# Optimization experiments

Hardware: AMD Instinct MI355X
Metric: run time of the kernel (lower is better)

The kernel has to match this reference:

```python
import jax, jax.numpy as jnp
import numpy as np

N = 50000          # nodes
E = 1600000        # edges (avg degree 32)
F_IN = 64          # input feature dim
SIZES = (64, 64)   # GATConv output sizes, heads=1
C_OUT = 5          # classifier classes
G = 64             # number of graphs in batch
SLOPE = 0.2        # LeakyReLU negative slope (PyG GATConv default)


def _glorot(key, shape):
    fan_in, fan_out = shape[0], shape[-1]
    s = jnp.sqrt(2.0 / (fan_in + fan_out)).astype(jnp.float32)
    return jax.random.normal(key, shape, jnp.float32) * s


def setup_inputs() -> dict:
    key = jax.random.key(0)
    ks = jax.random.split(key, 16)
    x = jax.random.normal(ks[0], (N, F_IN), jnp.float32)
    edge_index = jax.random.randint(ks[1], (2, E), 0, N)
    batch = jnp.sort(jax.random.randint(ks[2], (N,), 0, G))
    # layer 1 params
    W1 = _glorot(ks[3], (F_IN, SIZES[0]))
    a1s = _glorot(ks[4], (SIZES[0],))
    a1d = _glorot(ks[5], (SIZES[0],))
    b1 = jnp.zeros((SIZES[0],), jnp.float32)
    # layer 2 params
    W2 = _glorot(ks[6], (SIZES[0], SIZES[1]))
    a2s = _glorot(ks[7], (SIZES[1],))
    a2d = _glorot(ks[8], (SIZES[1],))
    b2 = jnp.zeros((SIZES[1],), jnp.float32)
    # final linear
    Wl = _glorot(ks[9], (SIZES[1], C_OUT))
    bl = jnp.zeros((C_OUT,), jnp.float32)
    return {"x": x, "edge_index": edge_index, "batch": batch,
            "W1": W1, "a1s": a1s, "a1d": a1d, "b1": b1,
            "W2": W2, "a2s": a2s, "a2d": a2d, "b2": b2,
            "Wl": Wl, "bl": bl}


def _gat_conv(h_in, W, a_src, a_dst, b, src, dst):
    # PyG GATConv, heads=1: h = W x; e_ij = LeakyReLU(a_src.h_j + a_dst.h_i)
    # alpha = softmax over edges grouped by destination i; out_i = sum alpha*h_j + b
    h = h_in @ W                                   # [N, F]
    e = jax.nn.leaky_relu((h @ a_src)[src] + (h @ a_dst)[dst], SLOPE)  # [E']
    m = jax.ops.segment_max(e, dst, num_segments=N)
    p = jnp.exp(e - m[dst])
    z = jax.ops.segment_sum(p, dst, num_segments=N)
    alpha = p / z[dst]                             # [E']
    out = jax.ops.segment_sum(h[src] * alpha[:, None], dst, num_segments=N)
    return out + b


def reference(x, edge_index, batch, W1, a1s, a1d, b1, W2, a2s, a2d, b2, Wl, bl):
    # add self-loops (PyG GATConv default add_self_loops=True)
    loop = jnp.arange(N, dtype=edge_index.dtype)
    src = jnp.concatenate([edge_index[0], loop])
    dst = jnp.concatenate([edge_index[1], loop])
    h = jax.nn.relu(_gat_conv(x, W1, a1s, a1d, b1, src, dst))
    h = jax.nn.relu(_gat_conv(h, W2, a2s, a2d, b2, src, dst))
    # global max pool per graph
    g = jax.ops.segment_max(h, batch, num_segments=G)   # [G, F]
    # dropout(p=0.3) is identity in eval mode
    return g @ Wl + bl
```

## Files before the change

### kernel.cpp

```cpp
#include <hip/hip_runtime.h>
#include <hip/hip_fp16.h>

#define N_NODES 50000
#define N_EDGES 1600000
#define F 64
#define G_GRAPHS 64
#define C_CLS 5
#define SLOPE 0.2f

#define NBUCKET ((N_NODES + 127) >> 7)
#define ACHUNK 4096
#define NCHUNKS ((N_EDGES + ACHUNK - 1) / ACHUNK)
#define CAP 8192
#define MAXCH 4
#define XPAD 68

__device__ __forceinline__ float lrelu(float x) { return fmaxf(x, SLOPE * x); }


__global__ __launch_bounds__(256) void count_matrix(const int* __restrict__ dst,
                                                    int* __restrict__ Cmat) {
    __shared__ int hist[NBUCKET];
    int tid = threadIdx.x;
    int c = blockIdx.x;
    for (int i = tid; i < NBUCKET; i += 256) hist[i] = 0;
    __syncthreads();
    int base = c * ACHUNK;
    int lim = min(ACHUNK, N_EDGES - base);
    for (int t = tid; t < lim; t += 256) atomicAdd(&hist[dst[base + t] >> 7], 1);
    __syncthreads();
    for (int i = tid; i < NBUCKET; i += 256)
        Cmat[c * NBUCKET + i] = hist[i];
}

__global__ __launch_bounds__(512) void scan_chunk_offsets(const int* __restrict__ Cmat,
                                                          int* __restrict__ Coff,
                                                          int* __restrict__ gcount) {
    __shared__ int sc[512];
    int tid = threadIdx.x;
    int b = blockIdx.x;
    int v = (tid < NCHUNKS) ? Cmat[tid * NBUCKET + b] : 0;
    sc[tid] = v;
    __syncthreads();
    for (int s = 1; s < 512; s <<= 1) {
        int t = (tid >= s) ? sc[tid - s] : 0;
        __syncthreads();
        sc[tid] += t;
        __syncthreads();
    }
    if (tid < NCHUNKS) Coff[b * NCHUNKS + tid] = sc[tid] - v;
    if (tid == 0) gcount[b] = sc[511];
}

__global__ __launch_bounds__(512) void bucket_scatter(
    const int* __restrict__ src, const int* __restrict__ dst,
    const int* __restrict__ Cmat, const int* __restrict__ Coff,
    const int* __restrict__ gcount, unsigned int* __restrict__ bedges) {
    __shared__ int cur[NBUCKET];
    __shared__ int dloc[NBUCKET];
    __shared__ int sc[512];
    __shared__ unsigned long long stage[ACHUNK];
    int tid = threadIdx.x;
    int c = blockIdx.x;
    int base = c * ACHUNK;
    int lim = min(ACHUNK, N_EDGES - base);
    int gb = (tid < NBUCKET) ? gcount[tid] : 0;
    sc[tid] = gb;
    __syncthreads();
    for (int s = 1; s < 512; s <<= 1) {
        int t = (tid >= s) ? sc[tid - s] : 0;
        __syncthreads();
        sc[tid] += t;
        __syncthreads();
    }
    int bbase = sc[tid] - gb;
    __syncthreads();
    int v = (tid < NBUCKET) ? Cmat[c * NBUCKET + tid] : 0;
    sc[tid] = v;
    __syncthreads();
    for (int s = 1; s < 512; s <<= 1) {
        int t = (tid >= s) ? sc[tid - s] : 0;
        __syncthreads();
        sc[tid] += t;
        __syncthreads();
    }
    if (tid < NBUCKET) {
        int loff = sc[tid] - v;
        cur[tid] = loff;
        dloc[tid] = bbase + Coff[tid * NCHUNKS + c] - loff;
    }
    __syncthreads();
    for (int t = tid; t < lim; t += 512) {
        int d = dst[base + t];
        int pos = atomicAdd(&cur[d >> 7], 1);
        stage[pos] = ((unsigned long long)(unsigned)d << 32) | (unsigned)src[base + t];
    }
    __syncthreads();
    for (int t = tid; t < lim; t += 512) {
        unsigned long long p = stage[t];
        int d = (int)(p >> 32);
        bedges[dloc[d >> 7] + t] =
            ((unsigned)(d & 127) << 17) | (unsigned)(p & 0x1ffffull);
    }
}

__global__ __launch_bounds__(512) void bucket_csr(
    const unsigned int* __restrict__ bedges, const int* __restrict__ gcount,
    int* __restrict__ row_ptr, int* __restrict__ csr_src) {
    __shared__ int hist[128];
    __shared__ int sc[128];
    __shared__ int loff[129];
    __shared__ int cur[128];
    __shared__ int scg[512];
    __shared__ int outs[CAP];
    int tid = threadIdx.x;
    int b = blockIdx.x;
    int nbase = b << 7;
    int nlocal = min(128, N_NODES - nbase);
    int gb = (tid < NBUCKET) ? gcount[tid] : 0;
    scg[tid] = gb;
    __syncthreads();
    for (int s = 1; s < 512; s <<= 1) {
        int t = (tid >= s) ? scg[tid - s] : 0;
        __syncthreads();
        scg[tid] += t;
        __syncthreads();
    }
    int cnt = min(gcount[b], CAP);
    int cbase = scg[b] - gcount[b];
    if (tid < 128) { hist[tid] = 0; cur[tid] = 0; }
    __syncthreads();
    for (int t = tid; t < cnt; t += 512)
        atomicAdd(&hist[(int)(bedges[cbase + t] >> 17)], 1);
    __syncthreads();
    if (tid < 128) sc[tid] = hist[tid];
    __syncthreads();
    for (int s = 1; s < 128; s <<= 1) {
        int t = (tid < 128 && tid >= s) ? sc[tid - s] : 0;
        __syncthreads();
        if (tid < 128) sc[tid] += t;
        __syncthreads();
    }
    if (tid < 128) loff[tid + 1] = sc[tid];
    if (tid == 0) loff[0] = 0;
    __syncthreads();
    for (int t = tid; t < cnt; t += 512) {
        unsigned int p = bedges[cbase + t];
        int dl = (int)(p >> 17);
        int r = atomicAdd(&cur[dl], 1);
        outs[loff[dl] + r] = (int)(p & 0x1ffffu);
    }
    __syncthreads();
    for (int t = tid; t < cnt; t += 512) csr_src[cbase + t] = outs[t];
    for (int i = tid; i < nlocal; i += 512) row_ptr[nbase + i] = cbase + loff[i];
    if (b == NBUCKET - 1 && tid == 0) row_ptr[N_NODES] = cbase + loff[nlocal];
}


__global__ __launch_bounds__(256) void gemm_sd_kernel(
    const float* __restrict__ X, const float* __restrict__ W,
    const float* __restrict__ a_s, const float* __restrict__ a_d,
    __half* __restrict__ Hh, float* __restrict__ S, float* __restrict__ D) {
    __shared__ float Wl[F][F];
    __shared__ float Xl[64][XPAD];
    __shared__ float as_l[F], ad_l[F];
    int tid = threadIdx.x;
    for (int i = tid; i < F * F; i += 256) Wl[i >> 6][i & 63] = W[i];
    if (tid < F) { as_l[tid] = a_s[tid]; ad_l[tid] = a_d[tid]; }
    int tile0 = blockIdx.x * 64;
    #pragma unroll
    for (int j = 0; j < 4; j++) {
        int q = tid + (j << 8);
        int row = q >> 4;
        int col = (q & 15) << 2;
        int gr = tile0 + row;
        float4 xv = make_float4(0.f, 0.f, 0.f, 0.f);
        if (gr < N_NODES) xv = *(const float4*)&X[gr * F + col];
        Xl[row][col + 0] = xv.x; Xl[row][col + 1] = xv.y;
        Xl[row][col + 2] = xv.z; Xl[row][col + 3] = xv.w;
    }
    __syncthreads();
    int rsub = tid >> 4;
    int cg = (tid & 15) << 2;
    float acc[4][4];
    #pragma unroll
    for (int i = 0; i < 4; i++)
        #pragma unroll
        for (int c = 0; c < 4; c++) acc[i][c] = 0.f;
    for (int k4 = 0; k4 < F; k4 += 4) {
        float4 w0 = *(const float4*)&Wl[k4 + 0][cg];
        float4 w1 = *(const float4*)&Wl[k4 + 1][cg];
        float4 w2 = *(const float4*)&Wl[k4 + 2][cg];
        float4 w3 = *(const float4*)&Wl[k4 + 3][cg];
        #pragma unroll
        for (int i = 0; i < 4; i++) {
            float4 xv = *(const float4*)&Xl[rsub + (i << 4)][k4];
            acc[i][0] = fmaf(xv.x, w0.x, acc[i][0]); acc[i][1] = fmaf(xv.x, w0.y, acc[i][1]);
            acc[i][2] = fmaf(xv.x, w0.z, acc[i][2]); acc[i][3] = fmaf(xv.x, w0.w, acc[i][3]);
            acc[i][0] = fmaf(xv.y, w1.x, acc[i][0]); acc[i][1] = fmaf(xv.y, w1.y, acc[i][1]);
            acc[i][2] = fmaf(xv.y, w1.z, acc[i][2]); acc[i][3] = fmaf(xv.y, w1.w, acc[i][3]);
            acc[i][0] = fmaf(xv.z, w2.x, acc[i][0]); acc[i][1] = fmaf(xv.z, w2.y, acc[i][1]);
            acc[i][2] = fmaf(xv.z, w2.z, acc[i][2]); acc[i][3] = fmaf(xv.z, w2.w, acc[i][3]);
            acc[i][0] = fmaf(xv.w, w3.x, acc[i][0]); acc[i][1] = fmaf(xv.w, w3.y, acc[i][1]);
            acc[i][2] = fmaf(xv.w, w3.z, acc[i][2]); acc[i][3] = fmaf(xv.w, w3.w, acc[i][3]);
        }
    }
    float as0 = as_l[cg], as1 = as_l[cg + 1], as2 = as_l[cg + 2], as3 = as_l[cg + 3];
    float ad0 = ad_l[cg], ad1 = ad_l[cg + 1], ad2 = ad_l[cg + 2], ad3 = ad_l[cg + 3];
    #pragma unroll
    for (int i = 0; i < 4; i++) {
        int row = tile0 + rsub + (i << 4);
        if (row >= N_NODES) continue;
        __half2 p0 = __floats2half2_rn(acc[i][0], acc[i][1]);
        __half2 p1 = __floats2half2_rn(acc[i][2], acc[i][3]);
        __half2* hp = (__half2*)&Hh[row * F + cg];
        hp[0] = p0; hp[1] = p1;
        float sp = acc[i][0] * as0 + acc[i][1] * as1 + acc[i][2] * as2 + acc[i][3] * as3;
        float dp = acc[i][0] * ad0 + acc[i][1] * ad1 + acc[i][2] * ad2 + acc[i][3] * ad3;
        #pragma unroll
        for (int o = 1; o < 16; o <<= 1) {
            sp += __shfl_xor(sp, o, 64);
            dp += __shfl_xor(dp, o, 64);
        }
        if ((tid & 15) == 0) { S[row] = sp; D[row] = dp; }
    }
}


struct F8 { float v0, v1, v2, v3, v4, v5, v6, v7; };
__device__ __forceinline__ F8 h8_unpack(float4 r) {
    F8 f;
    __half2 a01 = *reinterpret_cast<__half2*>(&r.x);
    __half2 a23 = *reinterpret_cast<__half2*>(&r.y);
    __half2 a45 = *reinterpret_cast<__half2*>(&r.z);
    __half2 a67 = *reinterpret_cast<__half2*>(&r.w);
    f.v0 = __low2float(a01); f.v1 = __high2float(a01);
    f.v2 = __low2float(a23); f.v3 = __high2float(a23);
    f.v4 = __low2float(a45); f.v5 = __high2float(a45);
    f.v6 = __low2float(a67); f.v7 = __high2float(a67);
    return f;
}

#define ACC8(P, G) do { \
    a0 = fmaf(P, (G).v0, a0); a1 = fmaf(P, (G).v1, a1); \
    a2 = fmaf(P, (G).v2, a2); a3 = fmaf(P, (G).v3, a3); \
    a4 = fmaf(P, (G).v4, a4); a5 = fmaf(P, (G).v5, a5); \
    a6 = fmaf(P, (G).v6, a6); a7 = fmaf(P, (G).v7, a7); } while (0)

__global__ __launch_bounds__(256) void agg_kernel(
    const __half* __restrict__ Hh, const float* __restrict__ S, const float* __restrict__ Dv,
    const int* __restrict__ row_ptr, const int* __restrict__ csr_src,
    const float* __restrict__ bias, float* __restrict__ OUT) {
    int lane = threadIdx.x & 63;
    int i = (blockIdx.x * blockDim.x + threadIdx.x) >> 6;
    if (i >= N_NODES) return;
    int start = row_ptr[i], end = row_ptr[i + 1];
    int deg = end - start;
    int nch = (deg + 63) >> 6;
    float d_i = Dv[i];
    float eself = lrelu(S[i] + d_i);
    int g  = lane >> 3;
    int fl = (lane & 7) << 3;
    float a0 = 0.f, a1 = 0.f, a2 = 0.f, a3 = 0.f;
    float a4 = 0.f, a5 = 0.f, a6 = 0.f, a7 = 0.f;
    float z;

    if (nch <= MAXCH) {
        int   sj_reg[MAXCH];
        float p_reg[MAXCH];
        float m = eself;
        #pragma unroll
        for (int c = 0; c < MAXCH; c++) {
            int j = start + (c << 6) + lane;
            bool v = (c < nch) && (j < end);
            int sj = v ? csr_src[j] : 0;
            float e = v ? lrelu(S[sj] + d_i) : -1e30f;
            sj_reg[c] = sj;
            p_reg[c] = e;
            m = fmaxf(m, e);
        }
        #pragma unroll
        for (int o = 32; o > 0; o >>= 1) m = fmaxf(m, __shfl_xor(m, o, 64));
        float zlane = 0.f;
        #pragma unroll
        for (int c = 0; c < MAXCH; c++) {
            if (c < nch) {
                float p = __expf(p_reg[c] - m);
                p_reg[c] = p;
                zlane += p;
            }
        }
        #pragma unroll
        for (int o = 32; o > 0; o >>= 1) zlane += __shfl_xor(zlane, o, 64);
        float pself = __expf(eself - m);
        z = zlane + pself;
        F8 hs = h8_unpack(*(const float4*)&Hh[i * F + fl]);
        if (g == 0) {
            a0 = pself * hs.v0; a1 = pself * hs.v1; a2 = pself * hs.v2; a3 = pself * hs.v3;
            a4 = pself * hs.v4; a5 = pself * hs.v5; a6 = pself * hs.v6; a7 = pself * hs.v7;
        }
        #pragma unroll
        for (int c = 0; c < MAXCH; c++) {
            if (c >= nch) break;
            int cnt = min(64, deg - (c << 6));
            int iters = (cnt + 7) >> 3;
            float pj0 = __shfl(p_reg[c], g, 64);
            int   sj0 = __shfl(sj_reg[c], g, 64);
            float4 v0 = *(const float4*)&Hh[sj0 * F + fl];
            for (int t = 1; t < iters; t++) {
                int slot = (t << 3) + g;
                float pj1 = __shfl(p_reg[c], slot, 64);
                int   sj1 = __shfl(sj_reg[c], slot, 64);
                float4 v1 = *(const float4*)&Hh[sj1 * F + fl];
                F8 gg = h8_unpack(v0);
                ACC8(pj0, gg);
                pj0 = pj1; v0 = v1;
            }
            F8 gg = h8_unpack(v0);
            ACC8(pj0, gg);
        }
    } else {
        float m = eself;
        for (int j = start + lane; j < end; j += 64)
            m = fmaxf(m, lrelu(S[csr_src[j]] + d_i));
        #pragma unroll
        for (int o = 32; o > 0; o >>= 1) m = fmaxf(m, __shfl_xor(m, o, 64));
        float pself = __expf(eself - m);
        float zlane = 0.f;
        F8 hs = h8_unpack(*(const float4*)&Hh[i * F + fl]);
        if (g == 0) {
            a0 = pself * hs.v0; a1 = pself * hs.v1; a2 = pself * hs.v2; a3 = pself * hs.v3;
            a4 = pself * hs.v4; a5 = pself * hs.v5; a6 = pself * hs.v6; a7 = pself * hs.v7;
        }
        for (int cb = start; cb < end; cb += 64) {
            int j = cb + lane;
            bool v = j < end;
            int sj = v ? csr_src[j] : 0;
            float p = v ? __expf(lrelu(S[sj] + d_i) - m) : 0.f;
            zlane += p;
            int cnt = min(64, end - cb);
            int iters = (cnt + 7) >> 3;
            for (int t = 0; t < iters; t++) {
                int slot = (t << 3) + g;
                float pj = __shfl(p, slot, 64);
                int  sjt = __shfl(sj, slot, 64);
                F8 gg = h8_unpack(*(const float4*)&Hh[sjt * F + fl]);
                ACC8(pj, gg);
            }
        }
        #pragma unroll
        for (int o = 32; o > 0; o >>= 1) zlane += __shfl_xor(zlane, o, 64);
        z = zlane + pself;
    }
    #pragma unroll
    for (int o = 8; o <= 32; o <<= 1) {
        a0 += __shfl_xor(a0, o, 64); a1 += __shfl_xor(a1, o, 64);
        a2 += __shfl_xor(a2, o, 64); a3 += __shfl_xor(a3, o, 64);
        a4 += __shfl_xor(a4, o, 64); a5 += __shfl_xor(a5, o, 64);
        a6 += __shfl_xor(a6, o, 64); a7 += __shfl_xor(a7, o, 64);
    }
    if (g == 0) {
        float rz = 1.0f / z;
        float4 b0 = *(const float4*)&bias[fl];
        float4 b1 = *(const float4*)&bias[fl + 4];
        float4 o0, o1;
        o0.x = fmaxf(a0 * rz + b0.x, 0.f);
        o0.y = fmaxf(a1 * rz + b0.y, 0.f);
        o0.z = fmaxf(a2 * rz + b0.z, 0.f);
        o0.w = fmaxf(a3 * rz + b0.w, 0.f);
        o1.x = fmaxf(a4 * rz + b1.x, 0.f);
        o1.y = fmaxf(a5 * rz + b1.y, 0.f);
        o1.z = fmaxf(a6 * rz + b1.z, 0.f);
        o1.w = fmaxf(a7 * rz + b1.w, 0.f);
        *(float4*)&OUT[i * F + fl] = o0;
        *(float4*)&OUT[i * F + fl + 4] = o1;
    }
}


__global__ __launch_bounds__(256) void pool_kernel(
    const float* __restrict__ H, const int* __restrict__ batch, float* __restrict__ gmax) {
    int lane = threadIdx.x & 63;
    int gw = (blockIdx.x * blockDim.x + threadIdx.x) >> 6;
    int nw = (gridDim.x * blockDim.x) >> 6;
    int per = (N_NODES + nw - 1) / nw;
    int s = gw * per;
    int e = min(N_NODES, s + per);
    if (s >= e) return;
    int curb = batch[s];
    float mx = H[s * F + lane];
    for (int i = s + 1; i < e; i++) {
        int b = batch[i];
        float v = H[i * F + lane];
        if (b != curb) {
            atomicMax((int*)&gmax[curb * F + lane], __float_as_int(mx));
            curb = b; mx = v;
        } else {
            mx = fmaxf(mx, v);
        }
    }
    atomicMax((int*)&gmax[curb * F + lane], __float_as_int(mx));
}


__global__ void final_kernel(const float* __restrict__ gmax, const float* __restrict__ Wl,
                             const float* __restrict__ bl, float* __restrict__ out) {
    int g = blockIdx.x;
    int c = threadIdx.x;
    if (c < C_CLS) {
        float acc = bl[c];
        #pragma unroll
        for (int f = 0; f < F; f++) acc = fmaf(gmax[g * F + f], Wl[f * C_CLS + c], acc);
        out[g * C_CLS + c] = acc;
    }
}


extern "C" void kernel_launch(void* const* d_in, const int* in_sizes, int n_in,
                              void* d_out, int out_size, void* d_ws, size_t ws_size,
                              hipStream_t stream) {
    const float* x    = (const float*)d_in[0];
    const int*   ei   = (const int*)d_in[1];
    const int*   batch= (const int*)d_in[2];
    const float* W1   = (const float*)d_in[3];
    const float* a1s  = (const float*)d_in[4];
    const float* a1d  = (const float*)d_in[5];
    const float* b1   = (const float*)d_in[6];
    const float* W2   = (const float*)d_in[7];
    const float* a2s  = (const float*)d_in[8];
    const float* a2d  = (const float*)d_in[9];
    const float* b2   = (const float*)d_in[10];
    const float* Wl   = (const float*)d_in[11];
    const float* bl   = (const float*)d_in[12];
    float* out = (float*)d_out;

    const int* src = ei;
    const int* dst = ei + N_EDGES;

    char* ws = (char*)d_ws;
    size_t off = 0;
    auto alloc = [&](size_t bytes) { size_t o = off; off += (bytes + 255) & ~(size_t)255; return o; };
    int*   row_ptr = (int*)(ws + alloc((size_t)(N_NODES + 1) * 4));
    int*   csr_src = (int*)(ws + alloc((size_t)N_EDGES * 4));
    char*  hAbed   = ws + alloc((size_t)N_NODES * F * 4);
    unsigned int* bedges = (unsigned int*)hAbed;
    __half* Hh     = (__half*)hAbed;
    char*  hBc     = ws + alloc((size_t)N_NODES * F * 4);
    float* hB      = (float*)hBc;
    int*   Cmat    = (int*)hBc;
    int*   Coff    = (int*)(hBc + ((size_t)NCHUNKS * NBUCKET * 4 + 255 & ~(size_t)255));
    float* Sv      = (float*)(ws + alloc((size_t)N_NODES * 4));
    float* Dv      = (float*)(ws + alloc((size_t)N_NODES * 4));
    float* gmax    = (float*)(ws + alloc((size_t)G_GRAPHS * F * 4));
    int*   gcount  = (int*)(ws + alloc((size_t)NBUCKET * 4));

    count_matrix<<<NCHUNKS, 256, 0, stream>>>(dst, Cmat);
    scan_chunk_offsets<<<NBUCKET, 512, 0, stream>>>(Cmat, Coff, gcount);
    bucket_scatter<<<NCHUNKS, 512, 0, stream>>>(src, dst, Cmat, Coff, gcount, bedges);
    bucket_csr<<<NBUCKET, 512, 0, stream>>>(bedges, gcount, row_ptr, csr_src);

    gemm_sd_kernel<<<(N_NODES + 63) / 64, 256, 0, stream>>>(x, W1, a1s, a1d, Hh, Sv, Dv);
    agg_kernel<<<(N_NODES * 64 + 255) / 256, 256, 0, stream>>>(Hh, Sv, Dv, row_ptr, csr_src, b1, hB);

    gemm_sd_kernel<<<(N_NODES + 63) / 64, 256, 0, stream>>>(hB, W2, a2s, a2d, Hh, Sv, Dv);
    agg_kernel<<<(N_NODES * 64 + 255) / 256, 256, 0, stream>>>(Hh, Sv, Dv, row_ptr, csr_src, b2, hB);

    hipMemsetAsync(gmax, 0, (size_t)G_GRAPHS * F * 4, stream);
    pool_kernel<<<512, 256, 0, stream>>>(hB, batch, gmax);
    final_kernel<<<G_GRAPHS, 64, 0, stream>>>(gmax, Wl, bl, out);
}
```

Measured before the change: 156.4 us.

## Fuse global max pool into second aggregation kernel and fold gmax zeroing

Layer-2 aggregation no longer writes its node features to global memory. Each block instead gathers its four nodes' outputs in shared memory, reduces them per graph, and issues atomicMax into the per-graph max buffer. Zeroing of that buffer moves into the second GEMM kernel, so the memset, the separate pool kernel and the round trip of the layer-2 features are removed. The cost is far more global atomics on a small set of addresses, which can contend, plus a block-wide sync in the aggregation kernel. count_matrix also goes from 256 to 512 threads per block.

```diff
diff --git a/kernel.cpp b/kernel.cpp
--- a/kernel.cpp
+++ b/kernel.cpp
@@ -18,18 +18,18 @@
 __device__ __forceinline__ float lrelu(float x) { return fmaxf(x, SLOPE * x); }
 
 
-__global__ __launch_bounds__(256) void count_matrix(const int* __restrict__ dst,
+__global__ __launch_bounds__(512) void count_matrix(const int* __restrict__ dst,
                                                     int* __restrict__ Cmat) {
     __shared__ int hist[NBUCKET];
     int tid = threadIdx.x;
     int c = blockIdx.x;
-    for (int i = tid; i < NBUCKET; i += 256) hist[i] = 0;
+    for (int i = tid; i < NBUCKET; i += 512) hist[i] = 0;
     __syncthreads();
     int base = c * ACHUNK;
     int lim = min(ACHUNK, N_EDGES - base);
-    for (int t = tid; t < lim; t += 256) atomicAdd(&hist[dst[base + t] >> 7], 1);
-    __syncthreads();
-    for (int i = tid; i < NBUCKET; i += 256)
+    for (int t = tid; t < lim; t += 512) atomicAdd(&hist[dst[base + t] >> 7], 1);
+    __syncthreads();
+    for (int i = tid; i < NBUCKET; i += 512)
         Cmat[c * NBUCKET + i] = hist[i];
 }
 
@@ -160,11 +160,15 @@
 __global__ __launch_bounds__(256) void gemm_sd_kernel(
     const float* __restrict__ X, const float* __restrict__ W,
     const float* __restrict__ a_s, const float* __restrict__ a_d,
-    __half* __restrict__ Hh, float* __restrict__ S, float* __restrict__ D) {
+    __half* __restrict__ Hh, float* __restrict__ S, float* __restrict__ D,
+    float* __restrict__ gmax0) {
     __shared__ float Wl[F][F];
     __shared__ float Xl[64][XPAD];
     __shared__ float as_l[F], ad_l[F];
     int tid = threadIdx.x;
+    if (gmax0 && blockIdx.x == 0) {
+        for (int i = tid; i < G_GRAPHS * F; i += 256) gmax0[i] = 0.f;
+    }
     for (int i = tid; i < F * F; i += 256) Wl[i >> 6][i & 63] = W[i];
     if (tid < F) { as_l[tid] = a_s[tid]; ad_l[tid] = a_d[tid]; }
     int tile0 = blockIdx.x * 64;
@@ -250,7 +254,10 @@
 __global__ __launch_bounds__(256) void agg_kernel(
     const __half* __restrict__ Hh, const float* __restrict__ S, const float* __restrict__ Dv,
     const int* __restrict__ row_ptr, const int* __restrict__ csr_src,
-    const float* __restrict__ bias, float* __restrict__ OUT) {
+    const float* __restrict__ bias, float* __restrict__ OUT,
+    const int* __restrict__ batch, float* __restrict__ gmax, int fuse_pool) {
+    __shared__ float pout[4][F];
+    __shared__ int   pbat[4];
     int lane = threadIdx.x & 63;
     int i = (blockIdx.x * blockDim.x + threadIdx.x) >> 6;
     if (i >= N_NODES) return;
@@ -359,11 +366,11 @@
         a4 += __shfl_xor(a4, o, 64); a5 += __shfl_xor(a5, o, 64);
         a6 += __shfl_xor(a6, o, 64); a7 += __shfl_xor(a7, o, 64);
     }
+    float4 o0, o1;
     if (g == 0) {
         float rz = 1.0f / z;
         float4 b0 = *(const float4*)&bias[fl];
         float4 b1 = *(const float4*)&bias[fl + 4];
-        float4 o0, o1;
         o0.x = fmaxf(a0 * rz + b0.x, 0.f);
         o0.y = fmaxf(a1 * rz + b0.y, 0.f);
         o0.z = fmaxf(a2 * rz + b0.z, 0.f);
@@ -372,34 +379,38 @@
         o1.y = fmaxf(a5 * rz + b1.y, 0.f);
         o1.z = fmaxf(a6 * rz + b1.z, 0.f);
         o1.w = fmaxf(a7 * rz + b1.w, 0.f);
-        *(float4*)&OUT[i * F + fl] = o0;
-        *(float4*)&OUT[i * F + fl + 4] = o1;
-    }
-}
-
-
-__global__ __launch_bounds__(256) void pool_kernel(
-    const float* __restrict__ H, const int* __restrict__ batch, float* __restrict__ gmax) {
-    int lane = threadIdx.x & 63;
-    int gw = (blockIdx.x * blockDim.x + threadIdx.x) >> 6;
-    int nw = (gridDim.x * blockDim.x) >> 6;
-    int per = (N_NODES + nw - 1) / nw;
-    int s = gw * per;
-    int e = min(N_NODES, s + per);
-    if (s >= e) return;
-    int curb = batch[s];
-    float mx = H[s * F + lane];
-    for (int i = s + 1; i < e; i++) {
-        int b = batch[i];
-        float v = H[i * F + lane];
-        if (b != curb) {
-            atomicMax((int*)&gmax[curb * F + lane], __float_as_int(mx));
-            curb = b; mx = v;
-        } else {
-            mx = fmaxf(mx, v);
-        }
-    }
-    atomicMax((int*)&gmax[curb * F + lane], __float_as_int(mx));
+    }
+    if (!fuse_pool) {
+        if (g == 0) {
+            *(float4*)&OUT[i * F + fl] = o0;
+            *(float4*)&OUT[i * F + fl + 4] = o1;
+        }
+    } else {
+        int wid = threadIdx.x >> 6;
+        if (g == 0) {
+            *(float4*)&pout[wid][fl] = o0;
+            *(float4*)&pout[wid][fl + 4] = o1;
+            if (lane == 0) pbat[wid] = batch[i];
+        }
+        __syncthreads();
+        if (threadIdx.x < F) {
+            int f = threadIdx.x;
+            int curb = pbat[0];
+            float mx = pout[0][f];
+            #pragma unroll
+            for (int r = 1; r < 4; r++) {
+                int b = pbat[r];
+                float v = pout[r][f];
+                if (b != curb) {
+                    atomicMax((int*)&gmax[curb * F + f], __float_as_int(mx));
+                    curb = b; mx = v;
+                } else {
+                    mx = fmaxf(mx, v);
+                }
+            }
+            atomicMax((int*)&gmax[curb * F + f], __float_as_int(mx));
+        }
+    }
 }
 
 
@@ -454,18 +465,18 @@
     float* gmax    = (float*)(ws + alloc((size_t)G_GRAPHS * F * 4));
     int*   gcount  = (int*)(ws + alloc((size_t)NBUCKET * 4));
 
-    count_matrix<<<NCHUNKS, 256, 0, stream>>>(dst, Cmat);
+    count_matrix<<<NCHUNKS, 512, 0, stream>>>(dst, Cmat);
     scan_chunk_offsets<<<NBUCKET, 512, 0, stream>>>(Cmat, Coff, gcount);
     bucket_scatter<<<NCHUNKS, 512, 0, stream>>>(src, dst, Cmat, Coff, gcount, bedges);
     bucket_csr<<<NBUCKET, 512, 0, stream>>>(bedges, gcount, row_ptr, csr_src);
 
-    gemm_sd_kernel<<<(N_NODES + 63) / 64, 256, 0, stream>>>(x, W1, a1s, a1d, Hh, Sv, Dv);
-    agg_kernel<<<(N_NODES * 64 + 255) / 256, 256, 0, stream>>>(Hh, Sv, Dv, row_ptr, csr_src, b1, hB);
-
-    gemm_sd_kernel<<<(N_NODES + 63) / 64, 256, 0, stream>>>(hB, W2, a2s, a2d, Hh, Sv, Dv);
-    agg_kernel<<<(N_NODES * 64 + 255) / 256, 256, 0, stream>>>(Hh, Sv, Dv, row_ptr, csr_src, b2, hB);
-
-    hipMemsetAsync(gmax, 0, (size_t)G_GRAPHS * F * 4, stream);
-    pool_kernel<<<512, 256, 0, stream>>>(hB, batch, gmax);
+    gemm_sd_kernel<<<(N_NODES + 63) / 64, 256, 0, stream>>>(x, W1, a1s, a1d, Hh, Sv, Dv, nullptr);
+    agg_kernel<<<(N_NODES * 64 + 255) / 256, 256, 0, stream>>>(Hh, Sv, Dv, row_ptr, csr_src, b1, hB,
+                                                               batch, gmax, 0);
+
+    gemm_sd_kernel<<<(N_NODES + 63) / 64, 256, 0, stream>>>(hB, W2, a2s, a2d, Hh, Sv, Dv, gmax);
+    agg_kernel<<<(N_NODES * 64 + 255) / 256, 256, 0, stream>>>(Hh, Sv, Dv, row_ptr, csr_src, b2, nullptr,
+                                                               batch, gmax, 1);
+
     final_kernel<<<G_GRAPHS, 64, 0, stream>>>(gmax, Wl, bl, out);
 }
```

Result: faster. 152.0 us (-2.8%).
